# Optimization experiments

Hardware: AMD Instinct MI355X
Metric: run time of the kernel (lower is better)

The kernel has to match this reference:

```python
import jax, jax.numpy as jnp
import numpy as np

V, D, L, H, T, B = 128, 256, 2, 4, 4096, 8
DK, DV = 128, 256           # key_dim=0.5*D, value_dim=1.0*D (fla GLA defaults)
HK, HV = DK // H, DV // H   # 32, 64
GLN = 16.0                  # gate_logit_normalizer
CH = 64                     # chunk size
EPS = 1e-5

def layernorm(x, w, b):
    mu = x.mean(-1, keepdims=True)
    var = ((x - mu) ** 2).mean(-1, keepdims=True)
    return (x - mu) * jax.lax.rsqrt(var + EPS) * w + b

def gla_chunk(q, k, v, gk, scale):
    # q,k,gk: [B,T,H,HK], v: [B,T,H,HV]; gk are per-key log decay gates (<=0)
    B_, T_, H_, dk = q.shape
    dv = v.shape[-1]
    N = T_ // CH
    def rs(x):
        d = x.shape[-1]
        return x.reshape(B_, N, CH, H_, d).transpose(0, 3, 1, 2, 4)  # [B,H,N,C,d]
    q, k, v, gk = rs(q), rs(k), rs(v), rs(gk)
    b = jnp.cumsum(gk, axis=3)                       # inclusive within-chunk cumlog decay
    q_s = q * jnp.exp(b) * scale
    k_i = k * jnp.exp(-b)                            # for intra-chunk attention
    k_e = k * jnp.exp(b[..., -1:, :] - b)            # decayed to chunk end, for state update
    mask = jnp.tril(jnp.ones((CH, CH), bool))
    att = jnp.einsum('bhncd,bhnmd->bhncm', q_s, k_i)
    att = jnp.where(mask, att, 0.0)
    o_intra = jnp.einsum('bhncm,bhnmd->bhncd', att, v)
    g_last = jnp.exp(b[..., -1, :])                  # [B,H,N,dk] full-chunk decay
    kv = jnp.einsum('bhncd,bhnce->bhnde', k_e, v)    # [B,H,N,dk,dv]
    def step(S, inp):
        qc, gl, kvc = inp
        o = jnp.einsum('bhcd,bhde->bhce', qc, S)
        return S * gl[..., None] + kvc, o
    S0 = jnp.zeros((B_, H_, dk, dv), q.dtype)
    xs = (jnp.moveaxis(q_s, 2, 0), jnp.moveaxis(g_last, 2, 0), jnp.moveaxis(kv, 2, 0))
    _, o_inter = jax.lax.scan(step, S0, xs)
    o = o_intra + jnp.moveaxis(o_inter, 0, 2)        # [B,H,N,C,dv]
    return o.transpose(0, 2, 3, 1, 4).reshape(B_, T_, H_, dv)

def gla_attn(x, wq, wk, wv, wg, gk_w1, gk_w2, gk_b2, gnorm_w, wo):
    B_, T_, _ = x.shape
    q = (x @ wq).reshape(B_, T_, H, HK)
    k = (x @ wk).reshape(B_, T_, H, HK)
    v = (x @ wv).reshape(B_, T_, H, HV)
    gk = jax.nn.log_sigmoid(x @ gk_w1 @ gk_w2 + gk_b2) / GLN
    gk = gk.reshape(B_, T_, H, HK)
    o = gla_chunk(q, k, v, gk, HK ** -0.5)           # [B,T,H,HV]
    g = (x @ wg).reshape(B_, T_, H, HV)
    rms = jax.lax.rsqrt((o * o).mean(-1, keepdims=True) + EPS)
    o = o * rms * gnorm_w * (g * jax.nn.sigmoid(g))  # FusedRMSNormSwishGate
    return o.reshape(B_, T_, DV) @ wo

def setup_inputs() -> dict:
    key = jax.random.key(0)
    ks = jax.random.split(key, 16)
    s = 0.02
    return {
        'tokens': jax.random.randint(ks[0], (B, T), 0, V),
        'embed': jax.random.normal(ks[1], (V, D)) * s,
        'ln_w': jnp.ones((L, D)), 'ln_b': jnp.zeros((L, D)),
        'wq': jax.random.normal(ks[2], (L, D, DK)) * s,
        'wk': jax.random.normal(ks[3], (L, D, DK)) * s,
        'wv': jax.random.normal(ks[4], (L, D, DV)) * s,
        'wg': jax.random.normal(ks[5], (L, D, DV)) * s,
        'gk_w1': jax.random.normal(ks[6], (L, D, 16)) * s,
        'gk_w2': jax.random.normal(ks[7], (L, 16, DK)) * s,
        'gk_b2': jnp.zeros((L, DK)),
        'gnorm_w': jnp.ones((L, HV)),
        'wo': jax.random.normal(ks[8], (L, DV, D)) * s,
        'mlp_w1': jax.random.normal(ks[9], (L, D, 2 * D)) * s,
        'mlp_b1': jnp.zeros((L, 2 * D)),
        'mlp_w2': jax.random.normal(ks[10], (L, 2 * D, D)) * s,
        'mlp_b2': jnp.zeros((L, D)),
        'head_w': jax.random.normal(ks[11], (D, V)) * s,
        'head_b': jnp.zeros((V,)),
    }

def reference(tokens, embed, ln_w, ln_b, wq, wk, wv, wg, gk_w1, gk_w2, gk_b2,
              gnorm_w, wo, mlp_w1, mlp_b1, mlp_w2, mlp_b2, head_w, head_b):
    x = embed[tokens]
    for i in range(L):
        h = layernorm(x, ln_w[i], ln_b[i])
        x = x + gla_attn(h, wq[i], wk[i], wv[i], wg[i], gk_w1[i], gk_w2[i],
                         gk_b2[i], gnorm_w[i], wo[i])
        h = layernorm(x, ln_w[i], ln_b[i])
        x = x + jax.nn.gelu(h @ mlp_w1[i] + mlp_b1[i], approximate=False) @ mlp_w2[i] + mlp_b2[i]
    return x @ head_w + head_b
```

## Files before the change

kernel.cpp:

```cpp
#include <hip/hip_runtime.h>
#include <hip/hip_bf16.h>
#include <math.h>

namespace {

constexpr int Bq = 8, Tq = 4096, Dq = 256, Lq = 2, Hq = 4;
constexpr int DKq = 128, DVq = 256, HKq = 32, HVq = 64;
constexpr int Nq = Tq / 64;
constexpr int Mq = Bq * Tq;
constexpr int SQ = 896;
constexpr float SCALEq = 0.17677669529663688f;
constexpr int WL = 1114112;

typedef __hip_bfloat16 bf16;
typedef __attribute__((ext_vector_type(8))) short bf16x8;
typedef __attribute__((ext_vector_type(4))) float f32x4;

__device__ __forceinline__ float b2f(bf16 x) { return __bfloat162float(x); }

__device__ __forceinline__ bf16x8 ld8(const bf16* p) { return *(const bf16x8*)p; }
__device__ __forceinline__ bf16x8 ld8(const float* p) {
  const float4* q4 = (const float4*)p;
  float4 a = q4[0], b = q4[1];
  float v[8] = {a.x, a.y, a.z, a.w, b.x, b.y, b.z, b.w};
  bf16x8 r;
#pragma unroll
  for (int i = 0; i < 8; i++) r[i] = __builtin_bit_cast(short, __float2bfloat16(v[i]));
  return r;
}

__device__ __forceinline__ int swzk(int k, int row) {
  return (k & ~63) | ((((k >> 3) & 7) ^ (row & 7)) << 3) | (k & 7);
}

__device__ __forceinline__ size_t fidx(int n, int k, int K) {
  int ct = n >> 7, nt = (n >> 4) & 7, lr = n & 15;
  int k0 = k >> 6, kk = (k >> 5) & 1, lg = (k >> 3) & 3, e = k & 7;
  int fi = ((ct * (K >> 6) + k0) * 2 + kk) * 8 + nt;
  return (size_t)fi * 512 + (lg * 16 + lr) * 8 + e;
}

__device__ __forceinline__ void wsplit2(float v, bf16* hi, bf16* lo) {
  bf16 h = __float2bfloat16(v);
  *hi = h; *lo = __float2bfloat16(v - b2f(h));
}

__global__ void k_wprep(const float* __restrict__ wq, const float* __restrict__ wk,
                        const float* __restrict__ wv, const float* __restrict__ wg,
                        const float* __restrict__ g1, const float* __restrict__ g2,
                        const float* __restrict__ wo, const float* __restrict__ m1,
                        const float* __restrict__ m2, const float* __restrict__ hw,
                        bf16* __restrict__ Wt) {
  int g = blockIdx.x * 256 + threadIdx.x;
  if (g >= 2 * 540672 + 32768) return;
  if (g < 2 * 540672) {
    int l = g / 540672, r = g % 540672;
    bf16* dst = Wt + (size_t)l * WL;
    if (r < 196608) {
      int k, nf; float v;
      if (r < 32768)       { int r2 = r;          k = r2 >> 7; nf = (r2 & 127);       v = wq[l*32768 + r2]; }
      else if (r < 65536)  { int r2 = r - 32768;  k = r2 >> 7; nf = 128 + (r2 & 127); v = wk[l*32768 + r2]; }
      else if (r < 131072) { int r2 = r - 65536;  k = r2 >> 8; nf = 256 + (r2 & 255); v = wv[l*65536 + r2]; }
      else                 { int r2 = r - 131072; k = r2 >> 8; nf = 512 + (r2 & 255); v = wg[l*65536 + r2]; }
      size_t fo = fidx(nf, k, 256);
      wsplit2(v, &dst[fo], &dst[229376 + fo]);
    } else if (r < 212992) {
      int r2 = r - 196608; int k = r2 >> 7, n = r2 & 127;
      float v = 0.f;
#pragma unroll
      for (int i = 0; i < 16; i++) v += g1[l*4096 + k*16 + i] * g2[l*2048 + i*128 + n];
      size_t fo = fidx(768 + n, k, 256);
      wsplit2(v, &dst[fo], &dst[229376 + fo]);
    } else if (r < 278528) {
      int r2 = r - 212992; int k = r2 >> 8, n = r2 & 255;
      size_t fo = fidx(n, k, 256);
      wsplit2(wo[l*65536 + r2], &dst[458752 + fo], &dst[524288 + fo]);
    } else if (r < 409600) {
      int r2 = r - 278528; int k = r2 >> 9, n = r2 & 511;
      size_t fo = fidx(n, k, 256);
      wsplit2(m1[l*131072 + r2], &dst[589824 + fo], &dst[720896 + fo]);
    } else {
      int r2 = r - 409600; int k = r2 >> 8, n = r2 & 255;
      size_t fo = fidx(n, k, 512);
      wsplit2(m2[l*131072 + r2], &dst[851968 + fo], &dst[983040 + fo]);
    }
  } else {
    int r2 = g - 2 * 540672; int k = r2 >> 7, n = r2 & 127;
    size_t fo = fidx(n, k, 256);
    wsplit2(hw[r2], &Wt[2228224 + fo], &Wt[2228224 + 32768 + fo]);
  }
}

__global__ void k_embed(const int* __restrict__ tok, const float* __restrict__ emb,
                        float* __restrict__ x) {
  int row = blockIdx.x, i = threadIdx.x;
  x[(size_t)row * Dq + i] = emb[(size_t)tok[row] * Dq + i];
}

__global__ void k_ln(const float* __restrict__ x, const float* __restrict__ w,
                     const float* __restrict__ bb, bf16* __restrict__ h) {
  int row = blockIdx.x, i = threadIdx.x;
  float v = x[(size_t)row * Dq + i];
  float s = v, s2 = v * v;
#pragma unroll
  for (int o = 32; o > 0; o >>= 1) { s += __shfl_down(s, o, 64); s2 += __shfl_down(s2, o, 64); }
  __shared__ float rs[4], rs2[4];
  if ((i & 63) == 0) { rs[i >> 6] = s; rs2[i >> 6] = s2; }
  __syncthreads();
  float sum = rs[0] + rs[1] + rs[2] + rs[3];
  float sum2 = rs2[0] + rs2[1] + rs2[2] + rs2[3];
  float mu = sum * (1.f / Dq);
  float var = fmaxf(sum2 * (1.f / Dq) - mu * mu, 0.f);
  float r = rsqrtf(var + 1e-5f);
  h[(size_t)row * Dq + i] = __float2bfloat16((v - mu) * r * w[i] + bb[i]);
}

template <typename AT, typename OT, int EPI, bool BIAS, bool ACC>
__global__ __launch_bounds__(256, 4) void k_mgemm7(const AT* __restrict__ A, int lda,
                                                   const bf16* __restrict__ Whf,
                                                   const bf16* __restrict__ Wlf,
                                                   const float* __restrict__ bias,
                                                   OT* __restrict__ C, int ldc, int K) {
  __shared__ __attribute__((aligned(16))) bf16 At[128 * 64];
  int tid = threadIdx.x;
  int lane = tid & 63, wave = tid >> 6;
  int lr = lane & 15, lg = lane >> 4;
  int wm = (wave >> 1) * 64, wn = (wave & 1) * 64;
  int row0 = blockIdx.x * 128;
  int ct = blockIdx.y, nk = K >> 6;
  f32x4 acc[4][4];
#pragma unroll
  for (int m = 0; m < 4; m++)
#pragma unroll
    for (int n = 0; n < 4; n++) acc[m][n] = (f32x4){0.f, 0.f, 0.f, 0.f};

  for (int k0 = 0; k0 < K; k0 += 64) {
    int k0i = k0 >> 6;
#pragma unroll
    for (int p = 0; p < 4; p++) {
      int cix = p * 256 + tid, r = cix >> 3, j = (cix & 7) * 8;
      bf16x8 v = ld8(A + (size_t)(row0 + r) * lda + k0 + j);
      *(bf16x8*)&At[r * 64 + swzk(j, r)] = v;
    }
    __syncthreads();
#pragma unroll
    for (int kk = 0; kk < 64; kk += 32) {
      int fb = ((ct * nk + k0i) * 2 + (kk >> 5)) * 8 + (wn >> 4);
      const bf16* bhp = Whf + (size_t)fb * 512 + lane * 8;
      const bf16* blp = Wlf + (size_t)fb * 512 + lane * 8;
      bf16x8 af[4], bh4[4], bl4[4];
#pragma unroll
      for (int n = 0; n < 4; n++) {
        bh4[n] = *(const bf16x8*)(bhp + n * 512);
        bl4[n] = *(const bf16x8*)(blp + n * 512);
      }
#pragma unroll
      for (int m = 0; m < 4; m++) {
        int ar = wm + m * 16 + lr;
        af[m] = *(bf16x8*)&At[ar * 64 + swzk(kk + lg * 8, ar)];
      }
#pragma unroll
      for (int m = 0; m < 4; m++)
#pragma unroll
        for (int n = 0; n < 4; n++) {
          acc[m][n] = __builtin_amdgcn_mfma_f32_16x16x32_bf16(af[m], bh4[n], acc[m][n], 0, 0, 0);
          acc[m][n] = __builtin_amdgcn_mfma_f32_16x16x32_bf16(af[m], bl4[n], acc[m][n], 0, 0, 0);
        }
    }
    __syncthreads();
  }
#pragma unroll
  for (int m = 0; m < 4; m++) {
#pragma unroll
    for (int n = 0; n < 4; n++) {
      int col = ct * 128 + wn + n * 16 + lr;
      int rowb = row0 + wm + m * 16 + lg * 4;
      float bv = BIAS ? bias[col] : 0.f;
#pragma unroll
      for (int j = 0; j < 4; j++) {
        float v = acc[m][n][j] + bv;
        if (EPI == 2) v = 0.5f * v * (1.f + erff(v * 0.70710678118654752f));
        if (EPI == 3 && col >= 768) {
          float t = v + bias[col - 768];
          v = (fminf(t, 0.f) - log1pf(expf(-fabsf(t)))) * (1.f / 16.f);
        }
        size_t oi = (size_t)(rowb + j) * ldc + col;
        if constexpr (ACC) C[oi] += v;
        else if constexpr (sizeof(OT) == 2) C[oi] = __float2bfloat16(v);
        else C[oi] = v;
      }
    }
  }
}

__global__ __launch_bounds__(256) void k_intra(bf16* QKVG,
                                               bf16* __restrict__ O,
                                               bf16* __restrict__ KVt,
                                               float* __restrict__ GL) {
  int blk = blockIdx.x;
  int n = blk & 63, h = (blk >> 6) & 3, b = blk >> 8;
  __shared__ __attribute__((aligned(16))) char smem[47488];
  float* bshT = (float*)smem;
  bf16*  kvS  = (bf16*)smem;
  float* glv  = (float*)(smem + 8448);
  bf16*  vT   = (bf16*)(smem + 8576);
  bf16*  kiAH = (bf16*)(smem + 17792);
  bf16*  kiAL = (bf16*)(smem + 22400);
  bf16*  qsH  = (bf16*)(smem + 27008);
  bf16*  qsL  = (bf16*)(smem + 32128);
  bf16*  kiBH = (bf16*)(smem + 37248);
  bf16*  kiBL = (bf16*)(smem + 42368);
  bf16*  aH   = (bf16*)(smem + 27008);
  bf16*  aL   = (bf16*)(smem + 36224);
  int tid = threadIdx.x;
  int lane = tid & 63, wave = tid >> 6;
  int lr = lane & 15, lg = lane >> 4;
  size_t tbase = (size_t)b * Tq + n * 64;
  int bh = b * Hq + h;

  {
    int c = tid >> 2, dc = (tid & 3) * 8;
    bf16x8 g8 = *(const bf16x8*)(QKVG + (tbase + c) * SQ + 768 + h * HKq + dc);
#pragma unroll
    for (int i = 0; i < 8; i++) bshT[(dc + i) * 66 + c] = b2f(__builtin_bit_cast(bf16, (short)g8[i]));
  }
  __syncthreads();
#pragma unroll
  for (int dd = 0; dd < 8; dd++) {
    int d = wave * 8 + dd;
    float v = bshT[d * 66 + lane];
#pragma unroll
    for (int o = 1; o < 64; o <<= 1) {
      float t = __shfl_up(v, (unsigned)o, 64);
      if (lane >= o) v += t;
    }
    bshT[d * 66 + lane] = v;
  }
  __syncthreads();
  if (tid < 32) {
    float g = expf(bshT[tid * 66 + 63]);
    glv[tid] = g;
    GL[(size_t)(bh * Nq + n) * 32 + tid] = g;
  }
  {
    int c = tid >> 2, dc = (tid & 3) * 8;
    size_t qoff = (tbase + c) * SQ + h * HKq + dc;
    bf16x8 q8 = *(const bf16x8*)(QKVG + qoff);
    bf16x8 k8 = *(const bf16x8*)(QKVG + qoff + 128);
    bf16x8 qh8, ql8, kh8, kl8;
#pragma unroll
    for (int i = 0; i < 8; i++) {
      float bv = bshT[(dc + i) * 66 + c];
      float qv = b2f(__builtin_bit_cast(bf16, (short)q8[i])) * expf(bv) * SCALEq;
      float kv = b2f(__builtin_bit_cast(bf16, (short)k8[i])) * expf(-bv);
      bf16 qh = __float2bfloat16(qv); bf16 ql = __float2bfloat16(qv - b2f(qh));
      bf16 kh = __float2bfloat16(kv); bf16 kl = __float2bfloat16(kv - b2f(kh));
      qh8[i] = __builtin_bit_cast(short, qh); ql8[i] = __builtin_bit_cast(short, ql);
      kh8[i] = __builtin_bit_cast(short, kh); kl8[i] = __builtin_bit_cast(short, kl);
      kiAH[(dc + i) * 72 + c] = kh; kiAL[(dc + i) * 72 + c] = kl;
    }
    *(bf16x8*)&qsH[c * 40 + dc] = qh8;
    *(bf16x8*)&qsL[c * 40 + dc] = ql8;
    *(bf16x8*)&kiBH[c * 40 + dc] = kh8;
    *(bf16x8*)&kiBL[c * 40 + dc] = kl8;
    *(bf16x8*)(QKVG + qoff) = qh8;
  }
#pragma unroll
  for (int p = 0; p < 2; p++) {
    int idx = p * 256 + tid;
    int c = idx & 63, ec = (idx >> 6) * 8;
    bf16x8 v8 = *(const bf16x8*)(QKVG + (tbase + c) * SQ + 256 + h * HVq + ec);
#pragma unroll
    for (int i = 0; i < 8; i++) vT[(ec + i) * 72 + c] = __builtin_bit_cast(bf16, (short)v8[i]);
  }
  __syncthreads();
  f32x4 accq[4];
#pragma unroll
  for (int t = 0; t < 4; t++) accq[t] = (f32x4){0.f, 0.f, 0.f, 0.f};
  {
    bf16x8 afh = *(bf16x8*)&qsH[(wave * 16 + lr) * 40 + lg * 8];
    bf16x8 afl = *(bf16x8*)&qsL[(wave * 16 + lr) * 40 + lg * 8];
#pragma unroll
    for (int t = 0; t < 4; t++) {
      bf16x8 bh = *(bf16x8*)&kiBH[(t * 16 + lr) * 40 + lg * 8];
      bf16x8 bl = *(bf16x8*)&kiBL[(t * 16 + lr) * 40 + lg * 8];
      accq[t] = __builtin_amdgcn_mfma_f32_16x16x32_bf16(afh, bh, accq[t], 0, 0, 0);
      accq[t] = __builtin_amdgcn_mfma_f32_16x16x32_bf16(afh, bl, accq[t], 0, 0, 0);
      accq[t] = __builtin_amdgcn_mfma_f32_16x16x32_bf16(afl, bh, accq[t], 0, 0, 0);
    }
  }
  __syncthreads();
#pragma unroll
  for (int t = 0; t < 4; t++)
#pragma unroll
    for (int j = 0; j < 4; j++) {
      int row = wave * 16 + lg * 4 + j;
      int col = t * 16 + lr;
      float v = (col <= row) ? accq[t][j] : 0.f;
      bf16 hi = __float2bfloat16(v);
      aH[row * 72 + col] = hi;
      aL[row * 72 + col] = __float2bfloat16(v - b2f(hi));
    }
  __syncthreads();
  f32x4 acco[4];
#pragma unroll
  for (int t = 0; t < 4; t++) acco[t] = (f32x4){0.f, 0.f, 0.f, 0.f};
#pragma unroll
  for (int ks = 0; ks < 2; ks++) {
    bf16x8 ah = *(bf16x8*)&aH[(wave * 16 + lr) * 72 + ks * 32 + lg * 8];
    bf16x8 al = *(bf16x8*)&aL[(wave * 16 + lr) * 72 + ks * 32 + lg * 8];
#pragma unroll
    for (int t = 0; t < 4; t++) {
      bf16x8 bfv = *(bf16x8*)&vT[(t * 16 + lr) * 72 + ks * 32 + lg * 8];
      acco[t] = __builtin_amdgcn_mfma_f32_16x16x32_bf16(ah, bfv, acco[t], 0, 0, 0);
      acco[t] = __builtin_amdgcn_mfma_f32_16x16x32_bf16(al, bfv, acco[t], 0, 0, 0);
    }
  }
#pragma unroll
  for (int t = 0; t < 4; t++)
#pragma unroll
    for (int j = 0; j < 4; j++) {
      int row = wave * 16 + lg * 4 + j, e = t * 16 + lr;
      O[(tbase + row) * DVq + h * HVq + e] = __float2bfloat16(acco[t][j]);
    }
  f32x4 acck[2];
  acck[0] = (f32x4){0.f, 0.f, 0.f, 0.f};
  acck[1] = (f32x4){0.f, 0.f, 0.f, 0.f};
#pragma unroll
  for (int ks = 0; ks < 2; ks++) {
    bf16x8 akh = *(bf16x8*)&kiAH[((wave >> 1) * 16 + lr) * 72 + ks * 32 + lg * 8];
    bf16x8 akl = *(bf16x8*)&kiAL[((wave >> 1) * 16 + lr) * 72 + ks * 32 + lg * 8];
#pragma unroll
    for (int t = 0; t < 2; t++) {
      bf16x8 bfv = *(bf16x8*)&vT[(((wave & 1) * 2 + t) * 16 + lr) * 72 + ks * 32 + lg * 8];
      acck[t] = __builtin_amdgcn_mfma_f32_16x16x32_bf16(akh, bfv, acck[t], 0, 0, 0);
      acck[t] = __builtin_amdgcn_mfma_f32_16x16x32_bf16(akl, bfv, acck[t], 0, 0, 0);
    }
  }
#pragma unroll
  for (int t = 0; t < 2; t++)
#pragma unroll
    for (int j = 0; j < 4; j++) {
      int d = (wave >> 1) * 16 + lg * 4 + j;
      int e = ((wave & 1) * 2 + t) * 16 + lr;
      kvS[d * 72 + e] = __float2bfloat16(acck[t][j] * glv[d]);
    }
  __syncthreads();
  size_t kbase = (size_t)(bh * Nq + n) * 2048;
  {
    int d = tid >> 3, cc = (tid & 7) * 8;
    *(bf16x8*)&KVt[kbase + d * 64 + cc] = *(bf16x8*)&kvS[d * 72 + cc];
  }
}

__global__ __launch_bounds__(256) void k_inter(const bf16* __restrict__ QKVG,
                                               const float* __restrict__ GL,
                                               const bf16* __restrict__ KVt,
                                               bf16* __restrict__ O) {
  int blk = blockIdx.x;
  int es = blk & 7, h = (blk >> 3) & 3, b = blk >> 5;
  int e0 = es * 8;
  __shared__ __attribute__((aligned(16))) bf16 kvl[64 * 32 * 8];
  __shared__ float gl[64 * 32];
  __shared__ float S[64 * 32 * 8];
  int tid = threadIdx.x;
  int bh = b * Hq + h;
  const float* glp = GL + (size_t)bh * Nq * 32;
#pragma unroll
  for (int p = 0; p < 8; p++) { int i = p * 256 + tid; gl[i] = glp[i]; }
  const bf16* kvp = KVt + (size_t)bh * Nq * 2048 + e0;
#pragma unroll
  for (int p = 0; p < 8; p++) {
    int c8 = p * 256 + tid;
    *(bf16x8*)&kvl[c8 * 8] = *(const bf16x8*)(kvp + (size_t)(c8 >> 5) * 2048 + (size_t)(c8 & 31) * 64);
  }
  __syncthreads();
  {
    int pe = tid & 7, pd = tid >> 3;
    float s = 0.f;
    for (int n = 0; n < 64; n++) {
      S[(n * 32 + pd) * 8 + pe] = s;
      s = s * gl[n * 32 + pd] + b2f(kvl[(n * 32 + pd) * 8 + pe]);
    }
  }
  __syncthreads();
  int c = tid >> 2, ep = tid & 3;
  for (int n = 0; n < 64; n++) {
    size_t tbase = (size_t)b * Tq + n * 64;
    const bf16* qp = QKVG + (tbase + c) * SQ + h * HKq;
    const float* Sp = &S[n * 256];
    float a0 = 0.f, a1 = 0.f;
#pragma unroll
    for (int j = 0; j < 4; j++) {
      bf16x8 q8 = *(const bf16x8*)(qp + j * 8);
#pragma unroll
      for (int i = 0; i < 8; i++) {
        float qf = b2f(__builtin_bit_cast(bf16, (short)q8[i]));
        int d = j * 8 + i;
        a0 += qf * Sp[d * 8 + ep];
        a1 += qf * Sp[d * 8 + ep + 4];
      }
    }
    size_t oi = (tbase + c) * DVq + h * HVq + e0 + ep;
    O[oi] = __float2bfloat16(b2f(O[oi]) + a0);
    O[oi + 4] = __float2bfloat16(b2f(O[oi + 4]) + a1);
  }
}

__global__ void k_gate(bf16* __restrict__ O, const bf16* __restrict__ QKVG,
                       const float* __restrict__ gnw) {
  int row = blockIdx.x, tid = threadIdx.x;
  int e = tid & 63;
  float o = b2f(O[(size_t)row * DVq + tid]);
  float s = o * o;
#pragma unroll
  for (int of = 32; of > 0; of >>= 1) s += __shfl_xor(s, of, 64);
  float r = rsqrtf(s * (1.f / 64.f) + 1e-5f);
  float g = b2f(QKVG[(size_t)row * SQ + 512 + tid]);
  float sw = g / (1.f + expf(-g));
  O[(size_t)row * DVq + tid] = __float2bfloat16(o * r * gnw[e] * sw);
}

}

extern "C" void kernel_launch(void* const* d_in, const int* in_sizes, int n_in,
                              void* d_out, int out_size, void* d_ws, size_t ws_size,
                              hipStream_t stream) {
  const int*   tok  = (const int*)d_in[0];
  const float* emb  = (const float*)d_in[1];
  const float* ln_w = (const float*)d_in[2];
  const float* ln_b = (const float*)d_in[3];
  const float* wq   = (const float*)d_in[4];
  const float* wk   = (const float*)d_in[5];
  const float* wv   = (const float*)d_in[6];
  const float* wg   = (const float*)d_in[7];
  const float* gkw1 = (const float*)d_in[8];
  const float* gkw2 = (const float*)d_in[9];
  const float* gkb2 = (const float*)d_in[10];
  const float* gnw  = (const float*)d_in[11];
  const float* wo   = (const float*)d_in[12];
  const float* mw1  = (const float*)d_in[13];
  const float* mb1  = (const float*)d_in[14];
  const float* mw2  = (const float*)d_in[15];
  const float* mb2  = (const float*)d_in[16];
  const float* hw   = (const float*)d_in[17];
  const float* hb   = (const float*)d_in[18];

  if (ws_size < 134217728u) return;
  char* w = (char*)d_ws;
  float* X    = (float*)w;
  bf16*  Ob   = (bf16*)(w + 33554432);
  bf16*  Hbf  = Ob;
  bf16*  QKVG = (bf16*)(w + 50331648);
  bf16*  KVt  = (bf16*)(w + 109051904);
  float* GLb  = (float*)(w + 117440512);
  bf16*  Wt   = (bf16*)(w + 117702656);
  bf16*  MLPH = QKVG;

  dim3 blk(256);
  k_wprep<<<4353, blk, 0, stream>>>(wq, wk, wv, wg, gkw1, gkw2, wo, mw1, mw2, hw, Wt);
  k_embed<<<Mq, blk, 0, stream>>>(tok, emb, X);

  for (int l = 0; l < Lq; l++) {
    const bf16* Wl = Wt + (size_t)l * WL;
    k_ln<<<Mq, blk, 0, stream>>>(X, ln_w + l * Dq, ln_b + l * Dq, Hbf);
    k_mgemm7<bf16, bf16, 3, false, false><<<dim3(256, 7), blk, 0, stream>>>(Hbf, 256, Wl, Wl + 229376, gkb2 + l * DKq, QKVG, SQ, 256);
    k_intra<<<Bq * Hq * Nq, blk, 0, stream>>>(QKVG, Ob, KVt, GLb);
    k_inter<<<Bq * Hq * 8, blk, 0, stream>>>(QKVG, GLb, KVt, Ob);
    k_gate<<<Mq, blk, 0, stream>>>(Ob, QKVG, gnw + l * HVq);
    k_mgemm7<bf16, float, 0, false, true><<<dim3(256, 2), blk, 0, stream>>>(Ob, 256, Wl + 458752, Wl + 524288, nullptr, X, 256, 256);
    k_ln<<<Mq, blk, 0, stream>>>(X, ln_w + l * Dq, ln_b + l * Dq, Hbf);
    k_mgemm7<bf16, bf16, 2, true, false><<<dim3(256, 4), blk, 0, stream>>>(Hbf, 256, Wl + 589824, Wl + 720896, mb1 + l * 2 * Dq, MLPH, 512, 256);
    k_mgemm7<bf16, float, 0, true, true><<<dim3(256, 2), blk, 0, stream>>>(MLPH, 512, Wl + 851968, Wl + 983040, mb2 + l * Dq, X, 256, 512);
  }
  k_mgemm7<float, float, 0, true, false><<<dim3(256, 1), blk, 0, stream>>>(X, 256, Wt + 2228224, Wt + 2228224 + 32768, hb, (float*)d_out, 128, 256);
}
```

Baseline: 673.4 us.

## Fuse gate/groupnorm into output GEMM A-load and stage full K=256 tiles

Removes the separate k_gate kernel by applying the per-head RMS norm and SiLU gate while the output-projection GEMM loads its A tile. It also restructures the GEMM to stage a 128x256 A tile in shared memory at once instead of 64-wide K slices, which cuts the number of barriers. The larger shared buffer (64KB) lowers occupancy, and launch bounds drop from 4 to 2 blocks. The gate math is recomputed for each column-tile block (blockIdx.y = 2), so it runs twice per row.

```diff
diff --git a/kernel.cpp b/kernel.cpp
--- a/kernel.cpp
+++ b/kernel.cpp
@@ -115,13 +115,15 @@
   h[(size_t)row * Dq + i] = __float2bfloat16((v - mu) * r * w[i] + bb[i]);
 }
 
-template <typename AT, typename OT, int EPI, bool BIAS, bool ACC>
-__global__ __launch_bounds__(256, 4) void k_mgemm7(const AT* __restrict__ A, int lda,
+template <typename AT, typename OT, int EPI, bool BIAS, bool ACC, bool GATEA>
+__global__ __launch_bounds__(256, 2) void k_mgemm8(const AT* __restrict__ A, int lda,
                                                    const bf16* __restrict__ Whf,
                                                    const bf16* __restrict__ Wlf,
                                                    const float* __restrict__ bias,
-                                                   OT* __restrict__ C, int ldc, int K) {
-  __shared__ __attribute__((aligned(16))) bf16 At[128 * 64];
+                                                   OT* __restrict__ C, int ldc, int K,
+                                                   const bf16* __restrict__ GQ,
+                                                   const float* __restrict__ gnw) {
+  __shared__ __attribute__((aligned(16))) bf16 At[128 * 256];
   int tid = threadIdx.x;
   int lane = tid & 63, wave = tid >> 6;
   int lr = lane & 15, lg = lane >> 4;
@@ -134,40 +136,58 @@
 #pragma unroll
     for (int n = 0; n < 4; n++) acc[m][n] = (f32x4){0.f, 0.f, 0.f, 0.f};
 
-  for (int k0 = 0; k0 < K; k0 += 64) {
-    int k0i = k0 >> 6;
-#pragma unroll
-    for (int p = 0; p < 4; p++) {
-      int cix = p * 256 + tid, r = cix >> 3, j = (cix & 7) * 8;
-      bf16x8 v = ld8(A + (size_t)(row0 + r) * lda + k0 + j);
-      *(bf16x8*)&At[r * 64 + swzk(j, r)] = v;
+  for (int kc = 0; kc < K; kc += 256) {
+    if (kc) __syncthreads();
+#pragma unroll
+    for (int p = 0; p < 16; p++) {
+      int cix = p * 256 + tid, r = cix >> 5, j = (cix & 31) * 8;
+      bf16x8 v = ld8(A + (size_t)(row0 + r) * lda + kc + j);
+      if constexpr (GATEA) {
+        float o[8]; float s = 0.f;
+#pragma unroll
+        for (int i = 0; i < 8; i++) { o[i] = b2f(__builtin_bit_cast(bf16, (short)v[i])); s += o[i] * o[i]; }
+        s += __shfl_xor(s, 1, 64); s += __shfl_xor(s, 2, 64); s += __shfl_xor(s, 4, 64);
+        float rr = rsqrtf(s * (1.f / 64.f) + 1e-5f);
+        bf16x8 g8 = *(const bf16x8*)(GQ + (size_t)(row0 + r) * SQ + 512 + j);
+#pragma unroll
+        for (int i = 0; i < 8; i++) {
+          float g = b2f(__builtin_bit_cast(bf16, (short)g8[i]));
+          float sw = g / (1.f + expf(-g));
+          v[i] = __builtin_bit_cast(short, __float2bfloat16(o[i] * rr * gnw[(j + i) & 63] * sw));
+        }
+      }
+      *(bf16x8*)&At[r * 256 + swzk(j, r)] = v;
     }
     __syncthreads();
 #pragma unroll
-    for (int kk = 0; kk < 64; kk += 32) {
-      int fb = ((ct * nk + k0i) * 2 + (kk >> 5)) * 8 + (wn >> 4);
-      const bf16* bhp = Whf + (size_t)fb * 512 + lane * 8;
-      const bf16* blp = Wlf + (size_t)fb * 512 + lane * 8;
-      bf16x8 af[4], bh4[4], bl4[4];
-#pragma unroll
-      for (int n = 0; n < 4; n++) {
-        bh4[n] = *(const bf16x8*)(bhp + n * 512);
-        bl4[n] = *(const bf16x8*)(blp + n * 512);
+    for (int k0l = 0; k0l < 256; k0l += 64) {
+      int k0 = kc + k0l;
+      int k0i = k0 >> 6;
+#pragma unroll
+      for (int kk = 0; kk < 64; kk += 32) {
+        int fb = ((ct * nk + k0i) * 2 + (kk >> 5)) * 8 + (wn >> 4);
+        const bf16* bhp = Whf + (size_t)fb * 512 + lane * 8;
+        const bf16* blp = Wlf + (size_t)fb * 512 + lane * 8;
+        bf16x8 af[4], bh4[4], bl4[4];
+#pragma unroll
+        for (int n = 0; n < 4; n++) {
+          bh4[n] = *(const bf16x8*)(bhp + n * 512);
+          bl4[n] = *(const bf16x8*)(blp + n * 512);
+        }
+#pragma unroll
+        for (int m = 0; m < 4; m++) {
+          int ar = wm + m * 16 + lr;
+          af[m] = *(bf16x8*)&At[ar * 256 + swzk(k0l + kk + lg * 8, ar)];
+        }
+#pragma unroll
+        for (int m = 0; m < 4; m++)
+#pragma unroll
+          for (int n = 0; n < 4; n++) {
+            acc[m][n] = __builtin_amdgcn_mfma_f32_16x16x32_bf16(af[m], bh4[n], acc[m][n], 0, 0, 0);
+            acc[m][n] = __builtin_amdgcn_mfma_f32_16x16x32_bf16(af[m], bl4[n], acc[m][n], 0, 0, 0);
+          }
       }
-#pragma unroll
-      for (int m = 0; m < 4; m++) {
-        int ar = wm + m * 16 + lr;
-        af[m] = *(bf16x8*)&At[ar * 64 + swzk(kk + lg * 8, ar)];
-      }
-#pragma unroll
-      for (int m = 0; m < 4; m++)
-#pragma unroll
-        for (int n = 0; n < 4; n++) {
-          acc[m][n] = __builtin_amdgcn_mfma_f32_16x16x32_bf16(af[m], bh4[n], acc[m][n], 0, 0, 0);
-          acc[m][n] = __builtin_amdgcn_mfma_f32_16x16x32_bf16(af[m], bl4[n], acc[m][n], 0, 0, 0);
-        }
-    }
-    __syncthreads();
+    }
   }
 #pragma unroll
   for (int m = 0; m < 4; m++) {
@@ -407,20 +427,6 @@
   }
 }
 
-__global__ void k_gate(bf16* __restrict__ O, const bf16* __restrict__ QKVG,
-                       const float* __restrict__ gnw) {
-  int row = blockIdx.x, tid = threadIdx.x;
-  int e = tid & 63;
-  float o = b2f(O[(size_t)row * DVq + tid]);
-  float s = o * o;
-#pragma unroll
-  for (int of = 32; of > 0; of >>= 1) s += __shfl_xor(s, of, 64);
-  float r = rsqrtf(s * (1.f / 64.f) + 1e-5f);
-  float g = b2f(QKVG[(size_t)row * SQ + 512 + tid]);
-  float sw = g / (1.f + expf(-g));
-  O[(size_t)row * DVq + tid] = __float2bfloat16(o * r * gnw[e] * sw);
-}
-
 }
 
 extern "C" void kernel_launch(void* const* d_in, const int* in_sizes, int n_in,
@@ -464,14 +470,13 @@
   for (int l = 0; l < Lq; l++) {
     const bf16* Wl = Wt + (size_t)l * WL;
     k_ln<<<Mq, blk, 0, stream>>>(X, ln_w + l * Dq, ln_b + l * Dq, Hbf);
-    k_mgemm7<bf16, bf16, 3, false, false><<<dim3(256, 7), blk, 0, stream>>>(Hbf, 256, Wl, Wl + 229376, gkb2 + l * DKq, QKVG, SQ, 256);
+    k_mgemm8<bf16, bf16, 3, false, false, false><<<dim3(256, 7), blk, 0, stream>>>(Hbf, 256, Wl, Wl + 229376, gkb2 + l * DKq, QKVG, SQ, 256, nullptr, nullptr);
     k_intra<<<Bq * Hq * Nq, blk, 0, stream>>>(QKVG, Ob, KVt, GLb);
     k_inter<<<Bq * Hq * 8, blk, 0, stream>>>(QKVG, GLb, KVt, Ob);
-    k_gate<<<Mq, blk, 0, stream>>>(Ob, QKVG, gnw + l * HVq);
-    k_mgemm7<bf16, float, 0, false, true><<<dim3(256, 2), blk, 0, stream>>>(Ob, 256, Wl + 458752, Wl + 524288, nullptr, X, 256, 256);
+    k_mgemm8<bf16, float, 0, false, true, true><<<dim3(256, 2), blk, 0, stream>>>(Ob, 256, Wl + 458752, Wl + 524288, nullptr, X, 256, 256, QKVG, gnw + l * HVq);
     k_ln<<<Mq, blk, 0, stream>>>(X, ln_w + l * Dq, ln_b + l * Dq, Hbf);
-    k_mgemm7<bf16, bf16, 2, true, false><<<dim3(256, 4), blk, 0, stream>>>(Hbf, 256, Wl + 589824, Wl + 720896, mb1 + l * 2 * Dq, MLPH, 512, 256);
-    k_mgemm7<bf16, float, 0, true, true><<<dim3(256, 2), blk, 0, stream>>>(MLPH, 512, Wl + 851968, Wl + 983040, mb2 + l * Dq, X, 256, 512);
-  }
-  k_mgemm7<float, float, 0, true, false><<<dim3(256, 1), blk, 0, stream>>>(X, 256, Wt + 2228224, Wt + 2228224 + 32768, hb, (float*)d_out, 128, 256);
-}
+    k_mgemm8<bf16, bf16, 2, true, false, false><<<dim3(256, 4), blk, 0, stream>>>(Hbf, 256, Wl + 589824, Wl + 720896, mb1 + l * 2 * Dq, MLPH, 512, 256, nullptr, nullptr);
+    k_mgemm8<bf16, float, 0, true, true, false><<<dim3(256, 2), blk, 0, stream>>>(MLPH, 512, Wl + 851968, Wl + 983040, mb2 + l * Dq, X, 256, 512, nullptr, nullptr);
+  }
+  k_mgemm8<float, float, 0, true, false, false><<<dim3(256, 1), blk, 0, stream>>>(X, 256, Wt + 2228224, Wt + 2228224 + 32768, hb, (float*)d_out, 128, 256, nullptr, nullptr);
+}
```

Result: slower. 701.2 us (+4.1%).
